# Kernel tuning notes

Measured on AMD Instinct MI355X. Metric: run time of the kernel, lower is better.

## Reference

```python
import jax, jax.numpy as jnp
import numpy as np

NUM_HEADS = 12
DROP_RATIO = 0.25
LN_EPS = 1e-5


def _layernorm(x, g, b):
    m = jnp.mean(x, axis=-1, keepdims=True)
    v = jnp.var(x, axis=-1, keepdims=True)
    return (x - m) * jax.lax.rsqrt(v + LN_EPS) * g + b


def setup_inputs() -> dict:
    key = jax.random.key(0)
    ks = jax.random.split(key, 12)
    B, N, C = 16, 785, 768
    H = 4 * C
    s = 0.02
    return {
        "x": jax.random.normal(ks[0], (B, N, C), dtype=jnp.float32),
        "ln1_g": jnp.ones((C,), jnp.float32),
        "ln1_b": jnp.zeros((C,), jnp.float32),
        "w_qkv": jax.random.normal(ks[1], (C, 3 * C), jnp.float32) * s,  # qkv_bias=False
        "w_proj": jax.random.normal(ks[2], (C, C), jnp.float32) * s,
        "b_proj": jnp.zeros((C,), jnp.float32),
        "ln2_g": jnp.ones((C,), jnp.float32),
        "ln2_b": jnp.zeros((C,), jnp.float32),
        "w_fc1": jax.random.normal(ks[3], (C, H), jnp.float32) * s,
        "b_fc1": jnp.zeros((H,), jnp.float32),
        "w_fc2": jax.random.normal(ks[4], (H, C), jnp.float32) * s,
        "b_fc2": jnp.zeros((C,), jnp.float32),
    }


def _block(x, ln1_g, ln1_b, w_qkv, w_proj, b_proj, ln2_g, ln2_b,
           w_fc1, b_fc1, w_fc2, b_fc2):
    B, N, C = x.shape
    Hh = NUM_HEADS
    Dh = C // Hh
    scale = Dh ** -0.5
    target = N - int(N * DROP_RATIO)  # kept KV length (incl. CLS)

    h = _layernorm(x, ln1_g, ln1_b)
    qkv = (h @ w_qkv).reshape(B, N, 3, Hh, Dh).transpose(2, 0, 3, 1, 4)
    q, k, v = qkv[0], qkv[1], qkv[2]  # each [B, H, N, Dh]

    # 'low' branch: L2-norm token scoring on non-CLS k tokens, keep top (target-1)
    rem_k = k[:, :, 1:, :]
    rem_v = v[:, :, 1:, :]
    scores = jnp.linalg.norm(rem_k, axis=-1) / Dh  # [B, H, N-1]
    _, idx = jax.lax.top_k(scores, target - 1)
    idx = jnp.sort(idx, axis=-1)  # restore original token order
    idx_e = idx[..., None]
    new_k = jnp.concatenate(
        [k[:, :, :1, :], jnp.take_along_axis(rem_k, idx_e, axis=2)], axis=2)
    new_v = jnp.concatenate(
        [v[:, :, :1, :], jnp.take_along_axis(rem_v, idx_e, axis=2)], axis=2)

    attn = jnp.einsum('bhnd,bhmd->bhnm', q, new_k) * scale
    attn = jax.nn.softmax(attn, axis=-1)
    o = jnp.einsum('bhnm,bhmd->bhnd', attn, new_v)
    o = o.transpose(0, 2, 1, 3).reshape(B, N, C)
    o = o @ w_proj + b_proj
    x = x + o  # drop_path = 0

    h2 = _layernorm(x, ln2_g, ln2_b)
    m = jax.nn.gelu(h2 @ w_fc1 + b_fc1, approximate=False) @ w_fc2 + b_fc2
    return x + m


def reference(x, ln1_g, ln1_b, w_qkv, w_proj, b_proj, ln2_g, ln2_b,
              w_fc1, b_fc1, w_fc2, b_fc2):
    return _block(x, ln1_g, ln1_b, w_qkv, w_proj, b_proj, ln2_g, ln2_b,
                  w_fc1, b_fc1, w_fc2, b_fc2)
```

## Files before the change

### kernel.cpp

```cpp
#include <hip/hip_runtime.h>

#define B_ 16
#define NTOK 785
#define C_ 768
#define HH 12
#define DH 64
#define BHN (B_*HH)
#define KVLEN 589
#define KVPAD 640
#define MROWS (B_*785)
#define HID 3072

typedef __bf16  bf16x8  __attribute__((ext_vector_type(8)));
typedef short   short4v __attribute__((ext_vector_type(4)));
typedef float   f32x4   __attribute__((ext_vector_type(4)));
typedef int     int4v   __attribute__((ext_vector_type(4)));
typedef unsigned short u16;
typedef signed char i8;

__device__ __forceinline__ u16 f2b(float f) {
  unsigned u = __builtin_bit_cast(unsigned, f);
  u = u + 0x7FFFu + ((u >> 16) & 1u);
  return (u16)(u >> 16);
}

#define SH_I8   (127.0f / 6.0f)
#define SW1_I8  (127.0f / 0.125f)
#define DEQ1    ((6.0f * 0.125f) / (127.0f * 127.0f))
#define SG_I8   (127.0f / 4.0f)
#define SW2_I8  (127.0f / 0.12f)
#define DEQ2    ((4.0f * 0.12f) / (127.0f * 127.0f))

__device__ __forceinline__ i8 f2i8(float v, float s) {
  float q = rintf(v * s);
  q = fminf(127.0f, fmaxf(-127.0f, q));
  return (i8)(int)q;
}

__device__ __forceinline__ float gelu_f(float x) {
  float ax = fabsf(x) * 0.70710678118654752f;
  float t  = __builtin_amdgcn_rcpf(1.0f + 0.3275911f * ax);
  float y  = t * (0.254829592f + t * (-0.284496736f + t * (1.421413741f +
             t * (-1.453152027f + t * 1.061405429f))));
  float er = 1.0f - y * __expf(-ax * ax);
  er = copysignf(er, x);
  return 0.5f * x * (1.0f + er);
}

#define AS1C(p) ((const __attribute__((address_space(1))) void*)(p))
#define AS3(p)  ((__attribute__((address_space(3))) void*)(p))
#define SWZ(row, g) ((row)*64 + ((((g) ^ ((row)&7))) << 3))
#define SWZ8B(row, g) ((row)*128 + ((((g) ^ ((row)&7))) << 4))

#define OFF_H   ((size_t)0)
#define OFF_KF  ((size_t)19292160)
#define OFF_QB  (OFF_KF + (size_t)38584320)
#define OFF_VB  (OFF_QB + (size_t)19292160)
#define OFF_KP  (OFF_VB + (size_t)19292160)
#define OFF_VP  (OFF_KP + (size_t)15728640)
#define OFF_OB  (OFF_VP + (size_t)15728640)
#define OFF_WQ  (OFF_OB + (size_t)19292160)
#define OFF_WP  (OFF_WQ + (size_t)3538944)
#define OFF_W1  (OFF_WP + (size_t)1179648)
#define OFF_W2  (OFF_W1 + (size_t)4718592)
#define OFF_SC  (OFF_W2 + (size_t)4718592)
#define OFF_IX  (OFF_SC + (size_t)602112)
#define OFF_G   OFF_KF

__global__ __launch_bounds__(256)
void transpose_cast(const float* __restrict__ w, u16* __restrict__ wt, int K, int N) {
  __shared__ float T[64][65];
  const int k0 = blockIdx.x * 64, n0 = blockIdx.y * 64;
  const int tid = threadIdx.x;
  const int cc = tid & 63, rr = tid >> 6;
#pragma unroll
  for (int i = 0; i < 16; ++i) {
    int r = rr + i * 4;
    T[r][cc] = w[(size_t)(k0 + r) * N + n0 + cc];
  }
  __syncthreads();
#pragma unroll
  for (int i = 0; i < 16; ++i) {
    int r = rr + i * 4;
    wt[(size_t)(n0 + r) * K + k0 + cc] = f2b(T[cc][r]);
  }
}

__global__ __launch_bounds__(256)
void transpose_quant(const float* __restrict__ w, i8* __restrict__ wt, int K, int N,
                     float scale) {
  __shared__ float T[64][65];
  const int k0 = blockIdx.x * 64, n0 = blockIdx.y * 64;
  const int tid = threadIdx.x;
  const int cc = tid & 63, rr = tid >> 6;
#pragma unroll
  for (int i = 0; i < 16; ++i) {
    int r = rr + i * 4;
    T[r][cc] = w[(size_t)(k0 + r) * N + n0 + cc];
  }
  __syncthreads();
#pragma unroll
  for (int i = 0; i < 16; ++i) {
    int r = rr + i * 4;
    wt[(size_t)(n0 + r) * K + k0 + cc] = f2i8(T[cc][r], scale);
  }
}

__global__ __launch_bounds__(256)
void ln_kernel(const float* __restrict__ x, const float* __restrict__ g,
               const float* __restrict__ b, u16* __restrict__ out) {
  const int row = blockIdx.x;
  const int tid = threadIdx.x;
  const float* xr = x + (size_t)row * C_;
  float v0 = xr[tid], v1 = xr[tid + 256], v2 = xr[tid + 512];
  float sum = v0 + v1 + v2;
  float sq  = v0 * v0 + v1 * v1 + v2 * v2;
#pragma unroll
  for (int o = 32; o > 0; o >>= 1) { sum += __shfl_xor(sum, o); sq += __shfl_xor(sq, o); }
  __shared__ float rs[4], rq[4];
  int w = tid >> 6;
  if ((tid & 63) == 0) { rs[w] = sum; rq[w] = sq; }
  __syncthreads();
  sum = rs[0] + rs[1] + rs[2] + rs[3];
  sq  = rq[0] + rq[1] + rq[2] + rq[3];
  float mean = sum * (1.0f / C_);
  float var  = sq * (1.0f / C_) - mean * mean;
  float rstd = rsqrtf(var + 1e-5f);
  u16* orow = out + (size_t)row * C_;
  orow[tid]       = f2b((v0 - mean) * rstd * g[tid]       + b[tid]);
  orow[tid + 256] = f2b((v1 - mean) * rstd * g[tid + 256] + b[tid + 256]);
  orow[tid + 512] = f2b((v2 - mean) * rstd * g[tid + 512] + b[tid + 512]);
}

__global__ __launch_bounds__(256)
void ln_kernel_i8(const float* __restrict__ x, const float* __restrict__ g,
                  const float* __restrict__ b, i8* __restrict__ out) {
  const int row = blockIdx.x;
  const int tid = threadIdx.x;
  const float* xr = x + (size_t)row * C_;
  float v0 = xr[tid], v1 = xr[tid + 256], v2 = xr[tid + 512];
  float sum = v0 + v1 + v2;
  float sq  = v0 * v0 + v1 * v1 + v2 * v2;
#pragma unroll
  for (int o = 32; o > 0; o >>= 1) { sum += __shfl_xor(sum, o); sq += __shfl_xor(sq, o); }
  __shared__ float rs[4], rq[4];
  int w = tid >> 6;
  if ((tid & 63) == 0) { rs[w] = sum; rq[w] = sq; }
  __syncthreads();
  sum = rs[0] + rs[1] + rs[2] + rs[3];
  sq  = rq[0] + rq[1] + rq[2] + rq[3];
  float mean = sum * (1.0f / C_);
  float var  = sq * (1.0f / C_) - mean * mean;
  float rstd = rsqrtf(var + 1e-5f);
  i8* orow = out + (size_t)row * C_;
  orow[tid]       = f2i8((v0 - mean) * rstd * g[tid]       + b[tid],       SH_I8);
  orow[tid + 256] = f2i8((v1 - mean) * rstd * g[tid + 256] + b[tid + 256], SH_I8);
  orow[tid + 512] = f2i8((v2 - mean) * rstd * g[tid + 512] + b[tid + 512], SH_I8);
}

template<int EPI>
__global__ __launch_bounds__(256, 2)
void gemm128(const u16* __restrict__ A, const u16* __restrict__ Bt,
             int M, int N, int K,
             const float* __restrict__ bias, const float* __restrict__ addsrc,
             float* __restrict__ outf, u16* __restrict__ outb,
             u16* __restrict__ qb, u16* __restrict__ kb, u16* __restrict__ vb,
             float* __restrict__ sc) {
  __shared__ u16 As[128 * 64];
  __shared__ u16 Bs[128 * 64];
  const int tid = threadIdx.x;
  const int lane = tid & 63;
  const int w = tid >> 6;
  const int wm = w >> 1, wn = w & 1;
  const int l15 = lane & 15;
  const int hi = lane >> 4;

  const int CN = (N + 127) >> 7;
  const int nwg = gridDim.x * gridDim.y;
  const int orig = blockIdx.x + blockIdx.y * gridDim.x;
  const int q = nwg >> 3, r8 = nwg & 7;
  const int xcd = orig & 7, pos = orig >> 3;
  const int wgid = (xcd < r8 ? xcd * (q + 1) : r8 * (q + 1) + (xcd - r8) * q) + pos;
  const int m0 = (wgid / CN) * 128;
  const int n0 = (wgid - (wgid / CN) * CN) * 128;

  const int srow = tid >> 3;
  const int sseg = tid & 7;

  f32x4 acc[4][4] = {};

  for (int kt = 0; kt < K; kt += 64) {
    __syncthreads();
#pragma unroll
    for (int i = 0; i < 4; ++i) {
      int row = i * 32 + srow;
      int gseg = sseg ^ (row & 7);
      int gr = m0 + row; if (gr >= M) gr = M - 1;
      int flat = i * 256 + tid;
      __builtin_amdgcn_global_load_lds(AS1C(A  + (size_t)gr * K         + kt + gseg * 8),
                                       AS3(&As[flat * 8]), 16, 0, 0);
      __builtin_amdgcn_global_load_lds(AS1C(Bt + (size_t)(n0 + row) * K + kt + gseg * 8),
                                       AS3(&Bs[flat * 8]), 16, 0, 0);
    }
    __syncthreads();
#pragma unroll
    for (int kk = 0; kk < 2; ++kk) {
      bf16x8 a[4], b[4];
#pragma unroll
      for (int mi = 0; mi < 4; ++mi)
        a[mi] = *reinterpret_cast<const bf16x8*>(&As[SWZ(wm * 64 + mi * 16 + l15, kk * 4 + hi)]);
#pragma unroll
      for (int ni = 0; ni < 4; ++ni)
        b[ni] = *reinterpret_cast<const bf16x8*>(&Bs[SWZ(wn * 64 + ni * 16 + l15, kk * 4 + hi)]);
#pragma unroll
      for (int mi = 0; mi < 4; ++mi)
#pragma unroll
        for (int ni = 0; ni < 4; ++ni)
          acc[mi][ni] = __builtin_amdgcn_mfma_f32_16x16x32_bf16(a[mi], b[ni], acc[mi][ni], 0, 0, 0);
    }
  }

#pragma unroll
  for (int mi = 0; mi < 4; ++mi) {
#pragma unroll
    for (int ni = 0; ni < 4; ++ni) {
#pragma unroll
      for (int j = 0; j < 4; ++j) {
        int r = m0 + wm * 64 + mi * 16 + hi * 4 + j;
        int c = n0 + wn * 64 + ni * 16 + l15;
        if (r < M) {
          float v = acc[mi][ni][j];
          if (EPI == 0) {
            int sec = (c >= 1536) ? 2 : (c >= 768 ? 1 : 0);
            int cm = c - sec * 768;
            int hh = cm >> 6, d = cm & 63;
            int bb = r / NTOK; int nn = r - bb * NTOK;
            size_t addr = (((size_t)(bb * HH + hh)) * NTOK + nn) * DH + d;
            if (sec == 0)      qb[addr] = f2b(v);
            else if (sec == 1) kb[addr] = f2b(v);
            else               vb[addr] = f2b(v);
          } else {
            size_t o = (size_t)r * N + c;
            outf[o] = v + bias[c] + addsrc[o];
          }
        }
      }
    }
  }

  if (EPI == 0) {
    int csec = n0 + wn * 64;
    if (csec >= 768 && csec < 1536) {
      int hh = (csec - 768) >> 6;
#pragma unroll
      for (int mi = 0; mi < 4; ++mi) {
#pragma unroll
        for (int j = 0; j < 4; ++j) {
          float ss = 0.0f;
#pragma unroll
          for (int ni = 0; ni < 4; ++ni) { float v = acc[mi][ni][j]; ss += v * v; }
          ss += __shfl_xor(ss, 1); ss += __shfl_xor(ss, 2);
          ss += __shfl_xor(ss, 4); ss += __shfl_xor(ss, 8);
          int r = m0 + wm * 64 + mi * 16 + hi * 4 + j;
          if (l15 == 0 && r < M) {
            int bb = r / NTOK, nn = r - bb * NTOK;
            if (nn >= 1)
              sc[(size_t)(bb * HH + hh) * 784 + nn - 1] = sqrtf(ss) * (1.0f / 64.0f);
          }
        }
      }
    }
  }
}

template<int EPI>
__global__ __launch_bounds__(256, 2)
void gemm128_i8(const i8* __restrict__ A, const i8* __restrict__ Bt,
                int M, int N, int K, float deq,
                const float* __restrict__ bias, const float* __restrict__ addsrc,
                float* __restrict__ outf, i8* __restrict__ outq) {
  __shared__ i8 As[128 * 128];
  __shared__ i8 Bs[128 * 128];
  const int tid = threadIdx.x;
  const int lane = tid & 63;
  const int w = tid >> 6;
  const int wm = w >> 1, wn = w & 1;
  const int l15 = lane & 15;
  const int hi = lane >> 4;

  const int CN = (N + 127) >> 7;
  const int nwg = gridDim.x * gridDim.y;
  const int orig = blockIdx.x + blockIdx.y * gridDim.x;
  const int q = nwg >> 3, r8 = nwg & 7;
  const int xcd = orig & 7, pos = orig >> 3;
  const int wgid = (xcd < r8 ? xcd * (q + 1) : r8 * (q + 1) + (xcd - r8) * q) + pos;
  const int m0 = (wgid / CN) * 128;
  const int n0 = (wgid - (wgid / CN) * CN) * 128;

  const int srow = tid >> 3;
  const int sg   = tid & 7;

  int4v acc[4][4] = {};

  for (int kt = 0; kt < K; kt += 128) {
    __syncthreads();
#pragma unroll
    for (int i = 0; i < 4; ++i) {
      int row = i * 32 + srow;
      int gsw = sg ^ (row & 7);
      int gr = m0 + row; if (gr >= M) gr = M - 1;
      int flat = i * 256 + tid;
      __builtin_amdgcn_global_load_lds(AS1C(A  + (size_t)gr * K         + kt + gsw * 16),
                                       AS3(&As[flat * 16]), 16, 0, 0);
      __builtin_amdgcn_global_load_lds(AS1C(Bt + (size_t)(n0 + row) * K + kt + gsw * 16),
                                       AS3(&Bs[flat * 16]), 16, 0, 0);
    }
    __syncthreads();
#pragma unroll
    for (int kk = 0; kk < 2; ++kk) {
      int4v a[4], b[4];
#pragma unroll
      for (int mi = 0; mi < 4; ++mi) {
        int R = wm * 64 + mi * 16 + l15;
        a[mi] = *reinterpret_cast<const int4v*>(&As[SWZ8B(R, kk * 4 + hi)]);
      }
#pragma unroll
      for (int ni = 0; ni < 4; ++ni) {
        int R = wn * 64 + ni * 16 + l15;
        b[ni] = *reinterpret_cast<const int4v*>(&Bs[SWZ8B(R, kk * 4 + hi)]);
      }
#pragma unroll
      for (int mi = 0; mi < 4; ++mi)
#pragma unroll
        for (int ni = 0; ni < 4; ++ni)
          acc[mi][ni] = __builtin_amdgcn_mfma_i32_16x16x64_i8(a[mi], b[ni], acc[mi][ni], 0, 0, 0);
    }
  }

#pragma unroll
  for (int mi = 0; mi < 4; ++mi) {
#pragma unroll
    for (int ni = 0; ni < 4; ++ni) {
#pragma unroll
      for (int j = 0; j < 4; ++j) {
        int r = m0 + wm * 64 + mi * 16 + hi * 4 + j;
        int c = n0 + wn * 64 + ni * 16 + l15;
        if (r < M) {
          float t = (float)acc[mi][ni][j] * deq + bias[c];
          if (EPI == 2) {
            outq[(size_t)r * N + c] = f2i8(gelu_f(t), SG_I8);
          } else {
            size_t o = (size_t)r * N + c;
            outf[o] = t + addsrc[o];
          }
        }
      }
    }
  }
}

__global__ __launch_bounds__(512)
void topk_kernel(const float* __restrict__ scores, int* __restrict__ idxb) {
  const int bh = blockIdx.x;
  const int tid = threadIdx.x;
  __shared__ float ss[1024];
  __shared__ int   sid[1024];
  __shared__ int   sid2[1024];
  for (int i = tid; i < 1024; i += 512) {
    ss[i]  = (i < 784) ? scores[bh * 784 + i] : -__builtin_inff();
    sid[i] = i;
  }
  for (int k = 2; k <= 1024; k <<= 1) {
    for (int j = k >> 1; j > 0; j >>= 1) {
      __syncthreads();
      for (int i = tid; i < 1024; i += 512) {
        int ixj = i ^ j;
        if (ixj > i) {
          float s1 = ss[i], s2 = ss[ixj];
          int   i1 = sid[i], i2 = sid[ixj];
          bool keep = (s1 > s2) || (s1 == s2 && i1 < i2);
          bool doSwap = ((i & k) == 0) ? !keep : keep;
          if (doSwap) { ss[i] = s2; ss[ixj] = s1; sid[i] = i2; sid[ixj] = i1; }
        }
      }
    }
  }
  __syncthreads();
  for (int i = tid; i < 1024; i += 512)
    sid2[i] = (i < 588) ? sid[i] : 0x7FFFFFFF;
  for (int k = 2; k <= 1024; k <<= 1) {
    for (int j = k >> 1; j > 0; j >>= 1) {
      __syncthreads();
      for (int i = tid; i < 1024; i += 512) {
        int ixj = i ^ j;
        if (ixj > i) {
          int a = sid2[i], b2 = sid2[ixj];
          bool keep = (a < b2);
          bool doSwap = ((i & k) == 0) ? !keep : keep;
          if (doSwap) { sid2[i] = b2; sid2[ixj] = a; }
        }
      }
    }
  }
  __syncthreads();
  for (int i = tid; i < 588; i += 512) idxb[bh * 588 + i] = sid2[i];
}

__global__ __launch_bounds__(256)
void gather_kernel(const u16* __restrict__ kb, const u16* __restrict__ vb,
                   const int* __restrict__ idxb, u16* __restrict__ kp, u16* __restrict__ vpT) {
  __shared__ u16 T[64 * 64];
  const int bh = blockIdx.x, chunk = blockIdx.y, t = threadIdx.x;
  {
    int jl = t >> 2, d0 = (t & 3) * 16;
    int j = chunk * 64 + jl;
    int n = (j == 0) ? 0 : (j <= 588 ? idxb[bh * 588 + j - 1] + 1 : -1);
    int4v k0 = {}, k1 = {}, v0 = {}, v1 = {};
    if (n >= 0) {
      size_t src = ((size_t)bh * NTOK + n) * DH + d0;
      k0 = *reinterpret_cast<const int4v*>(&kb[src]);
      k1 = *reinterpret_cast<const int4v*>(&kb[src + 8]);
      v0 = *reinterpret_cast<const int4v*>(&vb[src]);
      v1 = *reinterpret_cast<const int4v*>(&vb[src + 8]);
    }
    size_t kdst = ((size_t)bh * KVPAD + j) * DH + d0;
    *reinterpret_cast<int4v*>(&kp[kdst])     = k0;
    *reinterpret_cast<int4v*>(&kp[kdst + 8]) = k1;
    *reinterpret_cast<int4v*>(&T[jl * 64 + d0])     = v0;
    *reinterpret_cast<int4v*>(&T[jl * 64 + d0 + 8]) = v1;
  }
  __syncthreads();
  {
    int d = t & 63, kvo = (t >> 6) * 16;
    alignas(16) u16 tmp[16];
#pragma unroll
    for (int i = 0; i < 16; ++i) tmp[i] = T[(kvo + i) * 64 + d];
    size_t dst = ((size_t)bh * 64 + d) * KVPAD + chunk * 64 + kvo;
    *reinterpret_cast<int4v*>(&vpT[dst])     = *reinterpret_cast<int4v*>(&tmp[0]);
    *reinterpret_cast<int4v*>(&vpT[dst + 8]) = *reinterpret_cast<int4v*>(&tmp[8]);
  }
}

__global__ __launch_bounds__(256)
void attn_kernel(const u16* __restrict__ qb, const u16* __restrict__ kp,
                 const u16* __restrict__ vpT, u16* __restrict__ ob) {
  __shared__ u16 Qs[64 * 64];
  __shared__ u16 Ks[64 * 64];
  __shared__ u16 VTs[64 * 64];
  const int tid = threadIdx.x;
  const int lane = tid & 63;
  const int w = tid >> 6;
  const int l15 = lane & 15;
  const int hi = lane >> 4;

  const int nwg = gridDim.x;
  const int orig = blockIdx.x;
  const int q = nwg >> 3, r8 = nwg & 7;
  const int xcd = orig & 7, pos = orig >> 3;
  const int wgid = (xcd < r8 ? xcd * (q + 1) : r8 * (q + 1) + (xcd - r8) * q) + pos;
  const int bh = wgid / 13;
  const int n0 = (wgid - bh * 13) * 64;

#pragma unroll
  for (int i = 0; i < 2; ++i) {
    int flat = i * 256 + tid;
    int row = flat >> 3, g = flat & 7;
    int4v val = {};
    if (n0 + row < NTOK)
      val = *reinterpret_cast<const int4v*>(qb + ((size_t)bh * NTOK + n0 + row) * DH + g * 8);
    *reinterpret_cast<int4v*>(&Qs[SWZ(row, g)]) = val;
  }
  __syncthreads();
  bf16x8 q0 = *reinterpret_cast<const bf16x8*>(&Qs[SWZ(w * 16 + l15, hi)]);
  bf16x8 q1 = *reinterpret_cast<const bf16x8*>(&Qs[SWZ(w * 16 + l15, 4 + hi)]);

  float m_run = -__builtin_inff(), l_run = 0.0f;
  f32x4 oa[4] = {};

  for (int kvt = 0; kvt < 10; ++kvt) {
    int4v kr[2], vr[2];
#pragma unroll
    for (int i = 0; i < 2; ++i) {
      int flat = i * 256 + tid;
      int row = flat >> 3, g = flat & 7;
      kr[i] = *reinterpret_cast<const int4v*>(kp  + ((size_t)bh * KVPAD + kvt * 64 + row) * DH + g * 8);
      vr[i] = *reinterpret_cast<const int4v*>(vpT + ((size_t)bh * 64 + row) * KVPAD + kvt * 64 + g * 8);
    }
    __syncthreads();
#pragma unroll
    for (int i = 0; i < 2; ++i) {
      int flat = i * 256 + tid;
      int row = flat >> 3, g = flat & 7;
      *reinterpret_cast<int4v*>(&Ks[SWZ(row, g)])  = kr[i];
      *reinterpret_cast<int4v*>(&VTs[SWZ(row, g)]) = vr[i];
    }
    __syncthreads();

    f32x4 st[4];
#pragma unroll
    for (int ft = 0; ft < 4; ++ft) {
      bf16x8 a0 = *reinterpret_cast<const bf16x8*>(&Ks[SWZ(ft * 16 + l15, hi)]);
      bf16x8 a1 = *reinterpret_cast<const bf16x8*>(&Ks[SWZ(ft * 16 + l15, 4 + hi)]);
      f32x4 cfr = {};
      cfr = __builtin_amdgcn_mfma_f32_16x16x32_bf16(a0, q0, cfr, 0, 0, 0);
      cfr = __builtin_amdgcn_mfma_f32_16x16x32_bf16(a1, q1, cfr, 0, 0, 0);
      st[ft] = cfr;
    }
    float mx = -__builtin_inff();
#pragma unroll
    for (int ft = 0; ft < 4; ++ft) {
#pragma unroll
      for (int j = 0; j < 4; ++j) {
        int kv = kvt * 64 + ft * 16 + hi * 4 + j;
        float s = st[ft][j] * 0.125f;
        s = (kv < KVLEN) ? s : -__builtin_inff();
        st[ft][j] = s;
        mx = fmaxf(mx, s);
      }
    }
    mx = fmaxf(mx, __shfl_xor(mx, 16));
    mx = fmaxf(mx, __shfl_xor(mx, 32));
    float m_new = fmaxf(m_run, mx);
    float alpha = __expf(m_run - m_new);
    float psum = 0.0f;
    short4v pb[4];
#pragma unroll
    for (int ft = 0; ft < 4; ++ft) {
#pragma unroll
      for (int j = 0; j < 4; ++j) {
        float p = __expf(st[ft][j] - m_new);
        psum += p;
        pb[ft][j] = (short)f2b(p);
      }
    }
    psum += __shfl_xor(psum, 16);
    psum += __shfl_xor(psum, 32);
    l_run = l_run * alpha + psum;
    m_run = m_new;
#pragma unroll
    for (int df = 0; df < 4; ++df) {
      oa[df][0] *= alpha; oa[df][1] *= alpha; oa[df][2] *= alpha; oa[df][3] *= alpha;
    }
#pragma unroll
    for (int df = 0; df < 4; ++df) {
#pragma unroll
      for (int ft = 0; ft < 4; ++ft) {
        short4v va = *reinterpret_cast<const short4v*>(
            &VTs[SWZ(df * 16 + l15, ft * 2 + (hi >> 1)) + (hi & 1) * 4]);
        oa[df] = __builtin_amdgcn_mfma_f32_16x16x16bf16_1k(va, pb[ft], oa[df], 0, 0, 0);
      }
    }
  }
  int n = n0 + w * 16 + l15;
  if (n < NTOK) {
    float inv = 1.0f / l_run;
    int bb = bh / HH, hh = bh - bb * HH;
    size_t base = ((size_t)bb * NTOK + n) * C_ + hh * DH;
#pragma unroll
    for (int df = 0; df < 4; ++df) {
      short4v pv;
#pragma unroll
      for (int j = 0; j < 4; ++j) pv[j] = (short)f2b(oa[df][j] * inv);
      *reinterpret_cast<short4v*>(ob + base + df * 16 + hi * 4) = pv;
    }
  }
}

extern "C" void kernel_launch(void* const* d_in, const int* in_sizes, int n_in,
                              void* d_out, int out_size, void* d_ws, size_t ws_size,
                              hipStream_t stream) {
  const float* x     = (const float*)d_in[0];
  const float* ln1g  = (const float*)d_in[1];
  const float* ln1b  = (const float*)d_in[2];
  const float* wqkv  = (const float*)d_in[3];
  const float* wproj = (const float*)d_in[4];
  const float* bproj = (const float*)d_in[5];
  const float* ln2g  = (const float*)d_in[6];
  const float* ln2b  = (const float*)d_in[7];
  const float* wfc1  = (const float*)d_in[8];
  const float* bfc1  = (const float*)d_in[9];
  const float* wfc2  = (const float*)d_in[10];
  const float* bfc2  = (const float*)d_in[11];
  float* out = (float*)d_out;
  char* wsb = (char*)d_ws;

  u16*   h     = (u16*)(wsb + OFF_H);
  i8*    hq    = (i8*)(wsb + OFF_H);
  u16*   kb    = (u16*)(wsb + OFF_KF);
  u16*   qb    = (u16*)(wsb + OFF_QB);
  u16*   vb    = (u16*)(wsb + OFF_VB);
  u16*   kp    = (u16*)(wsb + OFF_KP);
  u16*   vpT   = (u16*)(wsb + OFF_VP);
  u16*   ob    = (u16*)(wsb + OFF_OB);
  u16*   wqT   = (u16*)(wsb + OFF_WQ);
  u16*   wpT   = (u16*)(wsb + OFF_WP);
  i8*    w1q   = (i8*)(wsb + OFF_W1);
  i8*    w2q   = (i8*)(wsb + OFF_W2);
  float* sc    = (float*)(wsb + OFF_SC);
  int*   idxb  = (int*)(wsb + OFF_IX);
  i8*    gq    = (i8*)(wsb + OFF_G);

  transpose_cast<<<dim3(768 / 64, 2304 / 64), 256, 0, stream>>>(wqkv, wqT, 768, 2304);
  transpose_cast<<<dim3(768 / 64, 768 / 64),  256, 0, stream>>>(wproj, wpT, 768, 768);
  transpose_quant<<<dim3(768 / 64, 3072 / 64), 256, 0, stream>>>(wfc1, w1q, 768, 3072, SW1_I8);
  transpose_quant<<<dim3(3072 / 64, 768 / 64), 256, 0, stream>>>(wfc2, w2q, 3072, 768, SW2_I8);

  ln_kernel<<<MROWS, 256, 0, stream>>>(x, ln1g, ln1b, h);

  gemm128<0><<<dim3(2304 / 128, 99), 256, 0, stream>>>(h, wqT, MROWS, 2304, 768,
      nullptr, nullptr, nullptr, nullptr, qb, kb, vb, sc);

  topk_kernel<<<BHN, 512, 0, stream>>>(sc, idxb);
  gather_kernel<<<dim3(BHN, KVPAD / 64), 256, 0, stream>>>(kb, vb, idxb, kp, vpT);

  attn_kernel<<<BHN * 13, 256, 0, stream>>>(qb, kp, vpT, ob);

  gemm128<1><<<dim3(768 / 128, 99), 256, 0, stream>>>(ob, wpT, MROWS, 768, 768,
      bproj, x, out, nullptr, nullptr, nullptr, nullptr, nullptr);

  ln_kernel_i8<<<MROWS, 256, 0, stream>>>(out, ln2g, ln2b, hq);

  gemm128_i8<2><<<dim3(3072 / 128, 99), 256, 0, stream>>>(hq, w1q, MROWS, 3072, 768,
      DEQ1, bfc1, nullptr, nullptr, gq);

  gemm128_i8<3><<<dim3(768 / 128, 99), 256, 0, stream>>>(gq, w2q, MROWS, 768, 3072,
      DEQ2, bfc2, out, out, nullptr);
}
```

Before: 391.9 us.

## Fold softmax scale into Q, use exp2, peel masked tile, swizzle V halves

The QKV epilogue now multiplies Q by scale*log2(e), so the attention loop can use exp2f directly without a per-score multiply. The KV loop is split into nine unmasked steps and one masked final step, which removes the per-element bounds check from most tiles. P is converted to bf16 by truncation instead of round-to-nearest. The V transpose writes 4-element halves in swizzled order, matched by an XOR in the LDS read, to reduce bank conflicts. Truncating P adds slight numerical bias, and the swizzle must stay consistent between the two kernels.

```diff
diff --git a/kernel.cpp b/kernel.cpp
--- a/kernel.cpp
+++ b/kernel.cpp
@@ -30,6 +30,8 @@
 #define SG_I8   (127.0f / 4.0f)
 #define SW2_I8  (127.0f / 0.12f)
 #define DEQ2    ((4.0f * 0.12f) / (127.0f * 127.0f))
+
+#define QSCALE  0.18033688011112042f
 
 __device__ __forceinline__ i8 f2i8(float v, float s) {
   float q = rintf(v * s);
@@ -236,7 +238,7 @@
             int hh = cm >> 6, d = cm & 63;
             int bb = r / NTOK; int nn = r - bb * NTOK;
             size_t addr = (((size_t)(bb * HH + hh)) * NTOK + nn) * DH + d;
-            if (sec == 0)      qb[addr] = f2b(v);
+            if (sec == 0)      qb[addr] = f2b(v * QSCALE);
             else if (sec == 1) kb[addr] = f2b(v);
             else               vb[addr] = f2b(v);
           } else {
@@ -432,9 +434,10 @@
   __syncthreads();
   {
     int d = t & 63, kvo = (t >> 6) * 16;
+    const int swp = ((d >> 3) & 1) * 4;
     alignas(16) u16 tmp[16];
 #pragma unroll
-    for (int i = 0; i < 16; ++i) tmp[i] = T[(kvo + i) * 64 + d];
+    for (int i = 0; i < 16; ++i) tmp[i ^ swp] = T[(kvo + i) * 64 + d];
     size_t dst = ((size_t)bh * 64 + d) * KVPAD + chunk * 64 + kvo;
     *reinterpret_cast<int4v*>(&vpT[dst])     = *reinterpret_cast<int4v*>(&tmp[0]);
     *reinterpret_cast<int4v*>(&vpT[dst + 8]) = *reinterpret_cast<int4v*>(&tmp[8]);
@@ -452,6 +455,7 @@
   const int w = tid >> 6;
   const int l15 = lane & 15;
   const int hi = lane >> 4;
+  const int hswp = (l15 >> 3) & 1;
 
   const int nwg = gridDim.x;
   const int orig = blockIdx.x;
@@ -477,80 +481,88 @@
   float m_run = -__builtin_inff(), l_run = 0.0f;
   f32x4 oa[4] = {};
 
-  for (int kvt = 0; kvt < 10; ++kvt) {
-    int4v kr[2], vr[2];
-#pragma unroll
-    for (int i = 0; i < 2; ++i) {
-      int flat = i * 256 + tid;
-      int row = flat >> 3, g = flat & 7;
-      kr[i] = *reinterpret_cast<const int4v*>(kp  + ((size_t)bh * KVPAD + kvt * 64 + row) * DH + g * 8);
-      vr[i] = *reinterpret_cast<const int4v*>(vpT + ((size_t)bh * 64 + row) * KVPAD + kvt * 64 + g * 8);
-    }
-    __syncthreads();
-#pragma unroll
-    for (int i = 0; i < 2; ++i) {
-      int flat = i * 256 + tid;
-      int row = flat >> 3, g = flat & 7;
-      *reinterpret_cast<int4v*>(&Ks[SWZ(row, g)])  = kr[i];
-      *reinterpret_cast<int4v*>(&VTs[SWZ(row, g)]) = vr[i];
-    }
-    __syncthreads();
-
-    f32x4 st[4];
-#pragma unroll
-    for (int ft = 0; ft < 4; ++ft) {
-      bf16x8 a0 = *reinterpret_cast<const bf16x8*>(&Ks[SWZ(ft * 16 + l15, hi)]);
-      bf16x8 a1 = *reinterpret_cast<const bf16x8*>(&Ks[SWZ(ft * 16 + l15, 4 + hi)]);
-      f32x4 cfr = {};
-      cfr = __builtin_amdgcn_mfma_f32_16x16x32_bf16(a0, q0, cfr, 0, 0, 0);
-      cfr = __builtin_amdgcn_mfma_f32_16x16x32_bf16(a1, q1, cfr, 0, 0, 0);
-      st[ft] = cfr;
-    }
-    float mx = -__builtin_inff();
-#pragma unroll
-    for (int ft = 0; ft < 4; ++ft) {
-#pragma unroll
-      for (int j = 0; j < 4; ++j) {
-        int kv = kvt * 64 + ft * 16 + hi * 4 + j;
-        float s = st[ft][j] * 0.125f;
-        s = (kv < KVLEN) ? s : -__builtin_inff();
-        st[ft][j] = s;
-        mx = fmaxf(mx, s);
-      }
-    }
-    mx = fmaxf(mx, __shfl_xor(mx, 16));
-    mx = fmaxf(mx, __shfl_xor(mx, 32));
-    float m_new = fmaxf(m_run, mx);
-    float alpha = __expf(m_run - m_new);
-    float psum = 0.0f;
-    short4v pb[4];
-#pragma unroll
-    for (int ft = 0; ft < 4; ++ft) {
-#pragma unroll
-      for (int j = 0; j < 4; ++j) {
-        float p = __expf(st[ft][j] - m_new);
-        psum += p;
-        pb[ft][j] = (short)f2b(p);
-      }
-    }
-    psum += __shfl_xor(psum, 16);
-    psum += __shfl_xor(psum, 32);
-    l_run = l_run * alpha + psum;
-    m_run = m_new;
-#pragma unroll
-    for (int df = 0; df < 4; ++df) {
-      oa[df][0] *= alpha; oa[df][1] *= alpha; oa[df][2] *= alpha; oa[df][3] *= alpha;
-    }
-#pragma unroll
-    for (int df = 0; df < 4; ++df) {
-#pragma unroll
-      for (int ft = 0; ft < 4; ++ft) {
-        short4v va = *reinterpret_cast<const short4v*>(
-            &VTs[SWZ(df * 16 + l15, ft * 2 + (hi >> 1)) + (hi & 1) * 4]);
-        oa[df] = __builtin_amdgcn_mfma_f32_16x16x16bf16_1k(va, pb[ft], oa[df], 0, 0, 0);
-      }
-    }
-  }
+#define ATTN_STEP(KVT, MASKED)                                                    \
+  {                                                                               \
+    int4v kr[2], vr[2];                                                           \
+    _Pragma("unroll")                                                             \
+    for (int i = 0; i < 2; ++i) {                                                 \
+      int flat = i * 256 + tid;                                                   \
+      int row = flat >> 3, g = flat & 7;                                          \
+      kr[i] = *reinterpret_cast<const int4v*>(                                    \
+          kp  + ((size_t)bh * KVPAD + (KVT) * 64 + row) * DH + g * 8);            \
+      vr[i] = *reinterpret_cast<const int4v*>(                                    \
+          vpT + ((size_t)bh * 64 + row) * KVPAD + (KVT) * 64 + g * 8);            \
+    }                                                                             \
+    __syncthreads();                                                              \
+    _Pragma("unroll")                                                             \
+    for (int i = 0; i < 2; ++i) {                                                 \
+      int flat = i * 256 + tid;                                                   \
+      int row = flat >> 3, g = flat & 7;                                          \
+      *reinterpret_cast<int4v*>(&Ks[SWZ(row, g)])  = kr[i];                       \
+      *reinterpret_cast<int4v*>(&VTs[SWZ(row, g)]) = vr[i];                       \
+    }                                                                             \
+    __syncthreads();                                                              \
+    f32x4 st[4];                                                                  \
+    _Pragma("unroll")                                                             \
+    for (int ft = 0; ft < 4; ++ft) {                                              \
+      bf16x8 a0 = *reinterpret_cast<const bf16x8*>(&Ks[SWZ(ft * 16 + l15, hi)]);  \
+      bf16x8 a1 = *reinterpret_cast<const bf16x8*>(&Ks[SWZ(ft * 16 + l15, 4 + hi)]); \
+      f32x4 cfr = {};                                                             \
+      cfr = __builtin_amdgcn_mfma_f32_16x16x32_bf16(a0, q0, cfr, 0, 0, 0);        \
+      cfr = __builtin_amdgcn_mfma_f32_16x16x32_bf16(a1, q1, cfr, 0, 0, 0);        \
+      if (MASKED) {                                                               \
+        _Pragma("unroll")                                                         \
+        for (int j = 0; j < 4; ++j) {                                             \
+          int kv = (KVT) * 64 + ft * 16 + hi * 4 + j;                             \
+          if (kv >= KVLEN) cfr[j] = -3.0e38f;                                     \
+        }                                                                         \
+      }                                                                           \
+      st[ft] = cfr;                                                               \
+    }                                                                             \
+    float mx = fmaxf(fmaxf(st[0][0], st[0][1]), fmaxf(st[0][2], st[0][3]));       \
+    _Pragma("unroll")                                                             \
+    for (int ft = 1; ft < 4; ++ft)                                                \
+      mx = fmaxf(mx, fmaxf(fmaxf(st[ft][0], st[ft][1]), fmaxf(st[ft][2], st[ft][3]))); \
+    mx = fmaxf(mx, __shfl_xor(mx, 16));                                           \
+    mx = fmaxf(mx, __shfl_xor(mx, 32));                                           \
+    float m_new = fmaxf(m_run, mx);                                               \
+    float alpha = exp2f(m_run - m_new);                                           \
+    float psum = 0.0f;                                                            \
+    short4v pb[4];                                                                \
+    _Pragma("unroll")                                                             \
+    for (int ft = 0; ft < 4; ++ft) {                                              \
+      _Pragma("unroll")                                                           \
+      for (int j = 0; j < 4; ++j) {                                               \
+        float p = exp2f(st[ft][j] - m_new);                                       \
+        psum += p;                                                                \
+        pb[ft][j] = (short)(u16)(__builtin_bit_cast(unsigned, p) >> 16);          \
+      }                                                                           \
+    }                                                                             \
+    psum += __shfl_xor(psum, 16);                                                 \
+    psum += __shfl_xor(psum, 32);                                                 \
+    l_run = l_run * alpha + psum;                                                 \
+    m_run = m_new;                                                                \
+    _Pragma("unroll")                                                             \
+    for (int df = 0; df < 4; ++df) {                                              \
+      oa[df][0] *= alpha; oa[df][1] *= alpha; oa[df][2] *= alpha; oa[df][3] *= alpha; \
+    }                                                                             \
+    _Pragma("unroll")                                                             \
+    for (int df = 0; df < 4; ++df) {                                              \
+      _Pragma("unroll")                                                           \
+      for (int ft = 0; ft < 4; ++ft) {                                            \
+        short4v va = *reinterpret_cast<const short4v*>(                           \
+            &VTs[SWZ(df * 16 + l15, ft * 2 + (hi >> 1)) + (((hi & 1) ^ hswp)) * 4]); \
+        oa[df] = __builtin_amdgcn_mfma_f32_16x16x16bf16_1k(va, pb[ft], oa[df], 0, 0, 0); \
+      }                                                                           \
+    }                                                                             \
+  }
+
+  for (int kvt = 0; kvt < 9; ++kvt) {
+    ATTN_STEP(kvt, false)
+  }
+  ATTN_STEP(9, true)
+#undef ATTN_STEP
+
   int n = n0 + w * 16 + l15;
   if (n < NTOK) {
     float inv = 1.0f / l_run;
```

Result: no change. 391.3 us (-0.2%).
